# Kernel tuning notes

Measured on AMD Instinct MI355X. Metric: run time of the kernel, lower is better.

Reference implementation:

```python
import jax, jax.numpy as jnp
import numpy as np

IN_CH, OUT_CH, Z1, B = 794, 512, 1024, 32768


def _build_masks(rng):
    # MADE connectivity masks, same construction as the torch module
    m0 = np.concatenate([np.ones(10, dtype=np.int64), np.arange(1, 785)])  # len 794
    m1 = rng.integers(1, IN_CH, size=Z1)
    m2 = rng.integers(m1.min(), IN_CH, size=OUT_CH)
    MW0 = (m1[:, None] >= m0[None, :IN_CH]).astype(np.float32)  # [Z1, IN_CH]
    MW1 = (m2[:, None] >= m1[None, :]).astype(np.float32)        # [OUT_CH, Z1]
    return jnp.asarray(MW0), jnp.asarray(MW1)


def setup_inputs() -> dict:
    key = jax.random.key(0)
    ks = jax.random.split(key, 9)
    s1 = 1.0 / np.sqrt(IN_CH)
    s2 = 1.0 / np.sqrt(Z1)
    MW0, MW1 = _build_masks(np.random.default_rng(0))
    return {
        "x":   jax.random.normal(ks[0], (B, IN_CH), dtype=jnp.float32),
        "W1":  jax.random.uniform(ks[1], (Z1, IN_CH), jnp.float32, -s1, s1),
        "b1":  jax.random.uniform(ks[2], (Z1,), jnp.float32, -s1, s1),
        "Wc1": jax.random.uniform(ks[3], (Z1, IN_CH), jnp.float32, -s1, s1),
        "bc1": jax.random.uniform(ks[4], (Z1,), jnp.float32, -s1, s1),
        "W2":  jax.random.uniform(ks[5], (OUT_CH, Z1), jnp.float32, -s2, s2),
        "b2":  jax.random.uniform(ks[6], (OUT_CH,), jnp.float32, -s2, s2),
        "Wc2": jax.random.uniform(ks[7], (OUT_CH, Z1), jnp.float32, -s2, s2),
        "bc2": jax.random.uniform(ks[8], (OUT_CH,), jnp.float32, -s2, s2),
        "MW0": MW0,
        "MW1": MW1,
    }


def reference(x, W1, b1, Wc1, bc1, W2, b2, Wc2, bc2, MW0, MW1):
    # F.linear(ones_like(x), Wc, bc) == row-sum of masked Wc + bc (same math, no GEMM)
    mW1, mWc1 = W1 * MW0, Wc1 * MW0
    h1 = jax.nn.relu(x @ mW1.T + b1 + jnp.sum(mWc1, axis=1) + bc1)  # [B, Z1]
    mW2, mWc2 = W2 * MW1, Wc2 * MW1
    h2 = jax.nn.relu(h1 @ mW2.T + b2 + jnp.sum(mWc2, axis=1) + bc2)  # [B, OUT_CH]
    return h2
```

## Files before the change

### kernel.cpp

```cpp
#include <hip/hip_runtime.h>
#include <hip/hip_bf16.h>
#include <stdint.h>

#define IN_CH 794
#define KPAD  832
#define Z1C   1024
#define OUT_C 512
#define BATCH 32768

typedef __attribute__((ext_vector_type(8))) short short8;
typedef __attribute__((ext_vector_type(4))) float f32x4;

__device__ __forceinline__ ushort f2bf(float f) {
  uint32_t u = __float_as_uint(f);
  return (ushort)((u + 0x7fffu + ((u >> 16) & 1u)) >> 16);
}

__device__ __forceinline__ void glds16(const void* g, void* l) {
  __builtin_amdgcn_global_load_lds(
      (const __attribute__((address_space(1))) void*)g,
      (__attribute__((address_space(3))) void*)l, 16, 0, 0);
}

#define BAR() __builtin_amdgcn_s_barrier()
#define MFMA(a, b, c) __builtin_amdgcn_mfma_f32_16x16x32_bf16(a, b, c, 0, 0, 0)

__global__ __launch_bounds__(256) void prep1(
    const float* __restrict__ W1, const float* __restrict__ b1,
    const float* __restrict__ Wc1, const float* __restrict__ bc1,
    const float* __restrict__ MW0, ushort* __restrict__ w1p,
    float* __restrict__ bias1) {
  int z = blockIdx.x, t = threadIdx.x;
  float sum = 0.f;
  for (int i = t; i < KPAD; i += 256) {
    float w = 0.f;
    if (i < IN_CH) {
      float m = MW0[z * IN_CH + i];
      w = W1[z * IN_CH + i] * m;
      sum += Wc1[z * IN_CH + i] * m;
    }
    w1p[z * KPAD + i] = f2bf(w);
  }
#pragma unroll
  for (int o = 32; o > 0; o >>= 1) sum += __shfl_down(sum, o, 64);
  __shared__ float red[4];
  if ((t & 63) == 0) red[t >> 6] = sum;
  __syncthreads();
  if (t == 0) bias1[z] = b1[z] + bc1[z] + red[0] + red[1] + red[2] + red[3];
}

__global__ __launch_bounds__(256) void prep2(
    const float* __restrict__ W2, const float* __restrict__ b2,
    const float* __restrict__ Wc2, const float* __restrict__ bc2,
    const float* __restrict__ MW1, ushort* __restrict__ w2m,
    float* __restrict__ bias2) {
  int z = blockIdx.x, t = threadIdx.x;
  float sum = 0.f;
  for (int i = t; i < Z1C; i += 256) {
    float m = MW1[z * Z1C + i];
    w2m[z * Z1C + i] = f2bf(W2[z * Z1C + i] * m);
    sum += Wc2[z * Z1C + i] * m;
  }
#pragma unroll
  for (int o = 32; o > 0; o >>= 1) sum += __shfl_down(sum, o, 64);
  __shared__ float red[4];
  if ((t & 63) == 0) red[t >> 6] = sum;
  __syncthreads();
  if (t == 0) bias2[z] = b2[z] + bc2[z] + red[0] + red[1] + red[2] + red[3];
}

__global__ __launch_bounds__(256) void xcvt(const float* __restrict__ x,
                                            ushort* __restrict__ xb) {
  const int CPR = KPAD / 8;
  const int total = BATCH * CPR;
  for (int i = blockIdx.x * 256 + threadIdx.x; i < total;
       i += gridDim.x * 256) {
    int row = i / CPR;
    int col = (i - row * CPR) * 8;
    const float* p = x + (size_t)row * IN_CH + col;
    ushort u[8];
    if (col + 8 <= IN_CH) {
#pragma unroll
      for (int j = 0; j < 4; ++j) {
        float2 v = *(const float2*)(p + j * 2);
        u[j * 2] = f2bf(v.x);
        u[j * 2 + 1] = f2bf(v.y);
      }
    } else {
#pragma unroll
      for (int j = 0; j < 8; ++j) u[j] = (col + j < IN_CH) ? f2bf(p[j]) : 0;
    }
    *(uint4*)(xb + (size_t)row * KPAD + col) = *(uint4*)u;
  }
}

template <int KP, int NKT, int NCB, int OSTR, bool BF16OUT>
__global__ __launch_bounds__(512, 2) void gemm8(
    const ushort* __restrict__ Ag, const ushort* __restrict__ Bg,
    const float* __restrict__ bias, void* __restrict__ Cout) {
  __shared__ ushort lds[73728];
  char* const L = (char*)lds;
  const int tid = threadIdx.x;
  const int lane = tid & 63, wid = tid >> 6;
  const int wr = wid >> 1, wc = wid & 1;

  const int nwg = gridDim.x;
  const int w0 = blockIdx.x;
  const int swz = (w0 & 7) * (nwg >> 3) + (w0 >> 3);
  const int bcol = (swz % NCB) * 128;
  const int brow = (swz / NCB) * 256;

  const int ra0 = tid >> 3;
  const int ra1 = 64 + (tid >> 3);
  const int cbs = (tid & 7) * 16;
  const size_t gA0 = (size_t)(brow + ra0) * (KP * 2) + (cbs ^ ((ra0 & 7) << 4));
  const size_t gA1 = (size_t)(brow + ra1) * (KP * 2) + (cbs ^ ((ra1 & 7) << 4));
  const int rb = tid >> 3;
  const size_t gB = (size_t)(bcol + rb) * (KP * 2) + (cbs ^ ((rb & 7) << 4));

  auto stA0 = [&](char* bufp, int kt, int h) {
    glds16((const char*)Ag + gA0 + (size_t)h * (128 * KP * 2) + (size_t)kt * 128,
           bufp + h * 16384 + wid * 1024);
  };
  auto stA1 = [&](char* bufp, int kt, int h) {
    glds16((const char*)Ag + gA1 + (size_t)h * (128 * KP * 2) + (size_t)kt * 128,
           bufp + h * 16384 + 8192 + wid * 1024);
  };
  auto stB = [&](char* bufp, int kt, int h) {
    glds16((const char*)Bg + gB + (size_t)h * (64 * KP * 2) + (size_t)kt * 128,
           bufp + 32768 + h * 8192 + wid * 1024);
  };

  const int rA = lane & 15;
  const int klo = (lane >> 4) * 16;
  const int xs = (rA & 7) << 4;

  f32x4 acc[4][4] = {};

  {
    char* b0 = L;
    stA0(b0, 0, 0); stA1(b0, 0, 0); stA0(b0, 0, 1); stA1(b0, 0, 1);
    stB(b0, 0, 0); stB(b0, 0, 1);
    char* b1 = L + 49152;
    stA0(b1, 1, 0); stA1(b1, 1, 0); stA0(b1, 1, 1); stA1(b1, 1, 1);
    stB(b1, 1, 0); stB(b1, 1, 1);
  }
  asm volatile("s_waitcnt vmcnt(6)" ::: "memory");
  BAR();

  for (int j = 0; j < NKT; ++j) {
    char* const Lb = L + (j % 3) * 49152;
    const bool pf = (j + 2 < NKT);
    char* const L2 = L + ((j + 2) % 3) * 49152;
    const int j2 = j + 2;

    auto rdA = [&](int m, int ks) -> short8 {
      int lrow = (wr & 1) * 64 + m * 16 + rA;
      return *(const short8*)(Lb + (wr >> 1) * 16384 + lrow * 128 +
                              ((ks * 64 + klo) ^ xs));
    };
    auto rdB = [&](int n, int ks) -> short8 {
      return *(const short8*)(Lb + 32768 + wc * 8192 + (n * 16 + rA) * 128 +
                              ((ks * 64 + klo) ^ xs));
    };

    short8 a0k0 = rdA(0, 0), a0k1 = rdA(0, 1);
    short8 a1k0 = rdA(1, 0), a1k1 = rdA(1, 1);
    short8 b0k0 = rdB(0, 0), b0k1 = rdB(0, 1);
    short8 b1k0 = rdB(1, 0), b1k1 = rdB(1, 1);
    if (pf) { stA0(L2, j2, 0); stA1(L2, j2, 0); }
    BAR();
    __builtin_amdgcn_s_setprio(1);
    acc[0][0] = MFMA(a0k0, b0k0, acc[0][0]); acc[0][0] = MFMA(a0k1, b0k1, acc[0][0]);
    acc[0][1] = MFMA(a0k0, b1k0, acc[0][1]); acc[0][1] = MFMA(a0k1, b1k1, acc[0][1]);
    acc[1][0] = MFMA(a1k0, b0k0, acc[1][0]); acc[1][0] = MFMA(a1k1, b0k1, acc[1][0]);
    acc[1][1] = MFMA(a1k0, b1k0, acc[1][1]); acc[1][1] = MFMA(a1k1, b1k1, acc[1][1]);
    __builtin_amdgcn_s_setprio(0);
    BAR();

    short8 b2k0 = rdB(2, 0), b2k1 = rdB(2, 1);
    short8 b3k0 = rdB(3, 0), b3k1 = rdB(3, 1);
    if (pf) { stA0(L2, j2, 1); stA1(L2, j2, 1); }
    BAR();
    __builtin_amdgcn_s_setprio(1);
    acc[0][2] = MFMA(a0k0, b2k0, acc[0][2]); acc[0][2] = MFMA(a0k1, b2k1, acc[0][2]);
    acc[0][3] = MFMA(a0k0, b3k0, acc[0][3]); acc[0][3] = MFMA(a0k1, b3k1, acc[0][3]);
    acc[1][2] = MFMA(a1k0, b2k0, acc[1][2]); acc[1][2] = MFMA(a1k1, b2k1, acc[1][2]);
    acc[1][3] = MFMA(a1k0, b3k0, acc[1][3]); acc[1][3] = MFMA(a1k1, b3k1, acc[1][3]);
    __builtin_amdgcn_s_setprio(0);
    BAR();

    short8 a2k0 = rdA(2, 0), a2k1 = rdA(2, 1);
    short8 a3k0 = rdA(3, 0), a3k1 = rdA(3, 1);
    if (pf) stB(L2, j2, 0);
    BAR();
    __builtin_amdgcn_s_setprio(1);
    acc[2][0] = MFMA(a2k0, b0k0, acc[2][0]); acc[2][0] = MFMA(a2k1, b0k1, acc[2][0]);
    acc[2][1] = MFMA(a2k0, b1k0, acc[2][1]); acc[2][1] = MFMA(a2k1, b1k1, acc[2][1]);
    acc[3][0] = MFMA(a3k0, b0k0, acc[3][0]); acc[3][0] = MFMA(a3k1, b0k1, acc[3][0]);
    acc[3][1] = MFMA(a3k0, b1k0, acc[3][1]); acc[3][1] = MFMA(a3k1, b1k1, acc[3][1]);
    __builtin_amdgcn_s_setprio(0);
    BAR();

    if (pf) {
      stB(L2, j2, 1);
      asm volatile("s_waitcnt vmcnt(6)" ::: "memory");
    } else if (j + 1 < NKT) {
      asm volatile("s_waitcnt vmcnt(0)" ::: "memory");
    }
    BAR();
    __builtin_amdgcn_s_setprio(1);
    acc[2][2] = MFMA(a2k0, b2k0, acc[2][2]); acc[2][2] = MFMA(a2k1, b2k1, acc[2][2]);
    acc[2][3] = MFMA(a2k0, b3k0, acc[2][3]); acc[2][3] = MFMA(a2k1, b3k1, acc[2][3]);
    acc[3][2] = MFMA(a3k0, b2k0, acc[3][2]); acc[3][2] = MFMA(a3k1, b2k1, acc[3][2]);
    acc[3][3] = MFMA(a3k0, b3k0, acc[3][3]); acc[3][3] = MFMA(a3k1, b3k1, acc[3][3]);
    __builtin_amdgcn_s_setprio(0);
    BAR();
  }

#pragma unroll
  for (int n = 0; n < 4; ++n) {
    const int col = bcol + wc * 64 + n * 16 + rA;
    const float bv = bias[col];
#pragma unroll
    for (int m = 0; m < 4; ++m) {
#pragma unroll
      for (int r = 0; r < 4; ++r) {
        const int row = brow + wr * 64 + m * 16 + (lane >> 4) * 4 + r;
        float v = acc[m][n][r] + bv;
        v = v > 0.f ? v : 0.f;
        if (BF16OUT)
          ((ushort*)Cout)[(size_t)row * OSTR + col] = f2bf(v);
        else
          ((float*)Cout)[(size_t)row * OSTR + col] = v;
      }
    }
  }
}

__global__ __launch_bounds__(256, 2) void gemm1_fused(
    const float* __restrict__ x, const ushort* __restrict__ w1p,
    const float* __restrict__ bias1, ushort* __restrict__ h1) {
  __shared__ ushort As[128 * 32];
  __shared__ ushort Bs[128 * 32];
  const int tid = threadIdx.x;
  const int lane = tid & 63, wid = tid >> 6;
  const int wr = wid >> 1, wc = wid & 1;
  const int brow = blockIdx.x * 128;
  const int bcol = blockIdx.y * 128;

  f32x4 acc[4][4] = {};
  const int arow = tid >> 1;
  const int acol0 = (tid & 1) * 16;
  const float* xrow = x + (size_t)(brow + arow) * IN_CH;

  for (int kt = 0; kt < 26; ++kt) {
    const int k0 = kt * 32;
#pragma unroll
    for (int c = 0; c < 2; ++c) {
      int idx16 = (wid * 2 + c) * 64 + lane;
      int row = idx16 >> 2, chunk = idx16 & 3;
      glds16(w1p + (size_t)(bcol + row) * KPAD + k0 + chunk * 8,
             (char*)Bs + (wid * 2 + c) * 1024);
    }
    union { ushort u[16]; uint4 q[2]; } pk;
    if (kt < 24) {
      const float* p = xrow + k0 + acol0;
#pragma unroll
      for (int j = 0; j < 8; ++j) {
        float2 v = *(const float2*)(p + j * 2);
        pk.u[j * 2] = f2bf(v.x);
        pk.u[j * 2 + 1] = f2bf(v.y);
      }
    } else {
#pragma unroll
      for (int j = 0; j < 16; ++j) {
        int col = k0 + acol0 + j;
        pk.u[j] = f2bf(col < IN_CH ? xrow[col] : 0.f);
      }
    }
    *(uint4*)&As[arow * 32 + acol0] = pk.q[0];
    *(uint4*)&As[arow * 32 + acol0 + 8] = pk.q[1];

    __syncthreads();
    const int kb = (lane >> 4) * 8, rA = lane & 15;
    short8 af[4], bfrag[4];
#pragma unroll
    for (int m = 0; m < 4; ++m)
      af[m] = *(const short8*)&As[(wr * 64 + m * 16 + rA) * 32 + kb];
#pragma unroll
    for (int n = 0; n < 4; ++n)
      bfrag[n] = *(const short8*)&Bs[(wc * 64 + n * 16 + rA) * 32 + kb];
#pragma unroll
    for (int m = 0; m < 4; ++m)
#pragma unroll
      for (int n = 0; n < 4; ++n)
        acc[m][n] = MFMA(af[m], bfrag[n], acc[m][n]);
    __syncthreads();
  }

  const int orow0 = brow + wr * 64;
  const int ocol0 = bcol + wc * 64;
#pragma unroll
  for (int n = 0; n < 4; ++n) {
    int col = ocol0 + n * 16 + (lane & 15);
    float bv = bias1[col];
#pragma unroll
    for (int m = 0; m < 4; ++m)
#pragma unroll
      for (int r = 0; r < 4; ++r) {
        int row = orow0 + m * 16 + (lane >> 4) * 4 + r;
        float v = acc[m][n][r] + bv;
        v = v > 0.f ? v : 0.f;
        h1[(size_t)row * Z1C + col] = f2bf(v);
      }
  }
}

extern "C" void kernel_launch(void* const* d_in, const int* in_sizes, int n_in,
                              void* d_out, int out_size, void* d_ws, size_t ws_size,
                              hipStream_t stream) {
  (void)in_sizes; (void)n_in; (void)out_size;
  const float* x   = (const float*)d_in[0];
  const float* W1  = (const float*)d_in[1];
  const float* b1  = (const float*)d_in[2];
  const float* Wc1 = (const float*)d_in[3];
  const float* bc1 = (const float*)d_in[4];
  const float* W2  = (const float*)d_in[5];
  const float* b2  = (const float*)d_in[6];
  const float* Wc2 = (const float*)d_in[7];
  const float* bc2 = (const float*)d_in[8];
  const float* MW0 = (const float*)d_in[9];
  const float* MW1 = (const float*)d_in[10];

  char* ws = (char*)d_ws;
  ushort* w1p   = (ushort*)ws;
  ushort* w2m   = (ushort*)(ws + 1703936);
  float*  bias1 = (float*)(ws + 2752512);
  float*  bias2 = (float*)(ws + 2756608);
  ushort* xb    = (ushort*)(ws + 2758656);
  const size_t WS_NEED = 2758656ull + 54525952ull;

  ushort* h1 = (ushort*)d_out;
  float*  out = (float*)d_out;

  prep1<<<1024, 256, 0, stream>>>(W1, b1, Wc1, bc1, MW0, w1p, bias1);
  prep2<<<512, 256, 0, stream>>>(W2, b2, Wc2, bc2, MW1, w2m, bias2);

  if (ws_size >= WS_NEED) {
    xcvt<<<2048, 256, 0, stream>>>(x, xb);
    gemm8<KPAD, 13, 8, Z1C, true><<<1024, 512, 0, stream>>>(xb, w1p, bias1, h1);
  } else {
    gemm1_fused<<<dim3(256, 8), 256, 0, stream>>>(x, w1p, bias1, h1);
  }
  gemm8<Z1C, 16, 4, OUT_C, false><<<512, 512, 0, stream>>>(h1, w2m, bias2, out);
}
```

Baseline: 140.1 us.

## Enlarge GEMM block tile to 256x256 with 2x4 warp layout and split buffering

Replaces the 256x128 block tile with a 256x256 tile, arranging 8 waves as 2x4 with each wave computing 128x64 (8x4 MFMA accumulators). A uses a triple-buffered LDS ring and B a double buffer, with loads interleaved into four compute phases. The aim is higher arithmetic intensity per LDS byte and fewer global reloads of operand tiles. In exchange it doubles accumulator registers and raises LDS use to 160KB, which may limit occupancy to one block per CU despite the launch bounds, and halves the grid size.

```diff
diff --git a/kernel.cpp b/kernel.cpp
--- a/kernel.cpp
+++ b/kernel.cpp
@@ -95,126 +95,137 @@
 }
 
 template <int KP, int NKT, int NCB, int OSTR, bool BF16OUT>
-__global__ __launch_bounds__(512, 2) void gemm8(
+__global__ __launch_bounds__(512, 2) void gemmT(
     const ushort* __restrict__ Ag, const ushort* __restrict__ Bg,
     const float* __restrict__ bias, void* __restrict__ Cout) {
-  __shared__ ushort lds[73728];
-  char* const L = (char*)lds;
+  __shared__ uint4 ldsq[10240];
+  char* const L = (char*)ldsq;
+  char* const LB = L + 98304;
   const int tid = threadIdx.x;
   const int lane = tid & 63, wid = tid >> 6;
-  const int wr = wid >> 1, wc = wid & 1;
+  const int wr = wid >> 2, wc = wid & 3;
 
   const int nwg = gridDim.x;
   const int w0 = blockIdx.x;
   const int swz = (w0 & 7) * (nwg >> 3) + (w0 >> 3);
-  const int bcol = (swz % NCB) * 128;
+  const int bcol = (swz % NCB) * 256;
   const int brow = (swz / NCB) * 256;
 
-  const int ra0 = tid >> 3;
-  const int ra1 = 64 + (tid >> 3);
-  const int cbs = (tid & 7) * 16;
-  const size_t gA0 = (size_t)(brow + ra0) * (KP * 2) + (cbs ^ ((ra0 & 7) << 4));
-  const size_t gA1 = (size_t)(brow + ra1) * (KP * 2) + (cbs ^ ((ra1 & 7) << 4));
-  const int rb = tid >> 3;
-  const size_t gB = (size_t)(bcol + rb) * (KP * 2) + (cbs ^ ((rb & 7) << 4));
-
-  auto stA0 = [&](char* bufp, int kt, int h) {
-    glds16((const char*)Ag + gA0 + (size_t)h * (128 * KP * 2) + (size_t)kt * 128,
-           bufp + h * 16384 + wid * 1024);
+  const int srow = tid >> 3;
+  const int scol = ((tid & 7) * 16) ^ ((srow & 7) << 4);
+  const char* gAp = (const char*)Ag + (size_t)(brow + srow) * (KP * 2) + scol;
+  const char* gBp = (const char*)Bg + (size_t)(bcol + srow) * (KP * 2) + scol;
+  const int ldst = wid * 1024;
+
+  auto stA = [&](int buf, int kt, int h) {
+    glds16(gAp + (size_t)h * (64 * KP * 2) + (size_t)kt * 128,
+           L + buf * 32768 + h * 8192 + ldst);
   };
-  auto stA1 = [&](char* bufp, int kt, int h) {
-    glds16((const char*)Ag + gA1 + (size_t)h * (128 * KP * 2) + (size_t)kt * 128,
-           bufp + h * 16384 + 8192 + wid * 1024);
-  };
-  auto stB = [&](char* bufp, int kt, int h) {
-    glds16((const char*)Bg + gB + (size_t)h * (64 * KP * 2) + (size_t)kt * 128,
-           bufp + 32768 + h * 8192 + wid * 1024);
+  auto stB = [&](int buf, int kt, int h) {
+    glds16(gBp + (size_t)h * (64 * KP * 2) + (size_t)kt * 128,
+           LB + buf * 32768 + h * 8192 + ldst);
   };
 
   const int rA = lane & 15;
   const int klo = (lane >> 4) * 16;
   const int xs = (rA & 7) << 4;
-
-  f32x4 acc[4][4] = {};
-
-  {
-    char* b0 = L;
-    stA0(b0, 0, 0); stA1(b0, 0, 0); stA0(b0, 0, 1); stA1(b0, 0, 1);
-    stB(b0, 0, 0); stB(b0, 0, 1);
-    char* b1 = L + 49152;
-    stA0(b1, 1, 0); stA1(b1, 1, 0); stA0(b1, 1, 1); stA1(b1, 1, 1);
-    stB(b1, 1, 0); stB(b1, 1, 1);
-  }
-  asm volatile("s_waitcnt vmcnt(6)" ::: "memory");
+  auto rdA = [&](const char* Ab, int m, int ks) -> short8 {
+    int row = wr * 128 + m * 16 + rA;
+    return *(const short8*)(Ab + row * 128 + ((ks * 64 + klo) ^ xs));
+  };
+  auto rdB = [&](const char* Bb, int n, int ks) -> short8 {
+    int row = wc * 64 + n * 16 + rA;
+    return *(const short8*)(Bb + row * 128 + ((ks * 64 + klo) ^ xs));
+  };
+
+  f32x4 acc[8][4] = {};
+
+#pragma unroll
+  for (int h = 0; h < 4; ++h) stA(0, 0, h);
+#pragma unroll
+  for (int h = 0; h < 4; ++h) stB(0, 0, h);
+#pragma unroll
+  for (int h = 0; h < 4; ++h) stA(1, 1, h);
+  asm volatile("s_waitcnt vmcnt(4)" ::: "memory");
   BAR();
 
   for (int j = 0; j < NKT; ++j) {
-    char* const Lb = L + (j % 3) * 49152;
-    const bool pf = (j + 2 < NKT);
-    char* const L2 = L + ((j + 2) % 3) * 49152;
-    const int j2 = j + 2;
-
-    auto rdA = [&](int m, int ks) -> short8 {
-      int lrow = (wr & 1) * 64 + m * 16 + rA;
-      return *(const short8*)(Lb + (wr >> 1) * 16384 + lrow * 128 +
-                              ((ks * 64 + klo) ^ xs));
-    };
-    auto rdB = [&](int n, int ks) -> short8 {
-      return *(const short8*)(Lb + 32768 + wc * 8192 + (n * 16 + rA) * 128 +
-                              ((ks * 64 + klo) ^ xs));
-    };
-
-    short8 a0k0 = rdA(0, 0), a0k1 = rdA(0, 1);
-    short8 a1k0 = rdA(1, 0), a1k1 = rdA(1, 1);
-    short8 b0k0 = rdB(0, 0), b0k1 = rdB(0, 1);
-    short8 b1k0 = rdB(1, 0), b1k1 = rdB(1, 1);
-    if (pf) { stA0(L2, j2, 0); stA1(L2, j2, 0); }
+    const char* Ab = L + (j % 3) * 32768;
+    const char* Bb = LB + (j & 1) * 32768;
+    const int jn = j + 1, ja = j + 2;
+    const int bb1 = jn & 1, ab2 = ja % 3;
+    short8 aF[4][2], bF[4][2];
+
+#pragma unroll
+    for (int m = 0; m < 4; ++m) {
+      aF[m][0] = rdA(Ab, m, 0); aF[m][1] = rdA(Ab, m, 1);
+    }
+#pragma unroll
+    for (int n = 0; n < 2; ++n) {
+      bF[n][0] = rdB(Bb, n, 0); bF[n][1] = rdB(Bb, n, 1);
+    }
+    if (jn < NKT) { stB(bb1, jn, 0); stB(bb1, jn, 1); }
     BAR();
     __builtin_amdgcn_s_setprio(1);
-    acc[0][0] = MFMA(a0k0, b0k0, acc[0][0]); acc[0][0] = MFMA(a0k1, b0k1, acc[0][0]);
-    acc[0][1] = MFMA(a0k0, b1k0, acc[0][1]); acc[0][1] = MFMA(a0k1, b1k1, acc[0][1]);
-    acc[1][0] = MFMA(a1k0, b0k0, acc[1][0]); acc[1][0] = MFMA(a1k1, b0k1, acc[1][0]);
-    acc[1][1] = MFMA(a1k0, b1k0, acc[1][1]); acc[1][1] = MFMA(a1k1, b1k1, acc[1][1]);
+#pragma unroll
+    for (int ks = 0; ks < 2; ++ks)
+#pragma unroll
+      for (int m = 0; m < 4; ++m)
+#pragma unroll
+        for (int n = 0; n < 2; ++n)
+          acc[m][n] = MFMA(aF[m][ks], bF[n][ks], acc[m][n]);
     __builtin_amdgcn_s_setprio(0);
     BAR();
 
-    short8 b2k0 = rdB(2, 0), b2k1 = rdB(2, 1);
-    short8 b3k0 = rdB(3, 0), b3k1 = rdB(3, 1);
-    if (pf) { stA0(L2, j2, 1); stA1(L2, j2, 1); }
+#pragma unroll
+    for (int n = 2; n < 4; ++n) {
+      bF[n][0] = rdB(Bb, n, 0); bF[n][1] = rdB(Bb, n, 1);
+    }
+    if (jn < NKT) { stB(bb1, jn, 2); stB(bb1, jn, 3); }
     BAR();
     __builtin_amdgcn_s_setprio(1);
-    acc[0][2] = MFMA(a0k0, b2k0, acc[0][2]); acc[0][2] = MFMA(a0k1, b2k1, acc[0][2]);
-    acc[0][3] = MFMA(a0k0, b3k0, acc[0][3]); acc[0][3] = MFMA(a0k1, b3k1, acc[0][3]);
-    acc[1][2] = MFMA(a1k0, b2k0, acc[1][2]); acc[1][2] = MFMA(a1k1, b2k1, acc[1][2]);
-    acc[1][3] = MFMA(a1k0, b3k0, acc[1][3]); acc[1][3] = MFMA(a1k1, b3k1, acc[1][3]);
+#pragma unroll
+    for (int ks = 0; ks < 2; ++ks)
+#pragma unroll
+      for (int m = 0; m < 4; ++m)
+#pragma unroll
+        for (int n = 2; n < 4; ++n)
+          acc[m][n] = MFMA(aF[m][ks], bF[n][ks], acc[m][n]);
     __builtin_amdgcn_s_setprio(0);
     BAR();
 
-    short8 a2k0 = rdA(2, 0), a2k1 = rdA(2, 1);
-    short8 a3k0 = rdA(3, 0), a3k1 = rdA(3, 1);
-    if (pf) stB(L2, j2, 0);
+#pragma unroll
+    for (int m = 0; m < 4; ++m) {
+      aF[m][0] = rdA(Ab, m + 4, 0); aF[m][1] = rdA(Ab, m + 4, 1);
+    }
+    if (ja < NKT) { stA(ab2, ja, 0); stA(ab2, ja, 1); }
     BAR();
     __builtin_amdgcn_s_setprio(1);
-    acc[2][0] = MFMA(a2k0, b0k0, acc[2][0]); acc[2][0] = MFMA(a2k1, b0k1, acc[2][0]);
-    acc[2][1] = MFMA(a2k0, b1k0, acc[2][1]); acc[2][1] = MFMA(a2k1, b1k1, acc[2][1]);
-    acc[3][0] = MFMA(a3k0, b0k0, acc[3][0]); acc[3][0] = MFMA(a3k1, b0k1, acc[3][0]);
-    acc[3][1] = MFMA(a3k0, b1k0, acc[3][1]); acc[3][1] = MFMA(a3k1, b1k1, acc[3][1]);
+#pragma unroll
+    for (int ks = 0; ks < 2; ++ks)
+#pragma unroll
+      for (int m = 0; m < 4; ++m)
+#pragma unroll
+        for (int n = 0; n < 2; ++n)
+          acc[m + 4][n] = MFMA(aF[m][ks], bF[n][ks], acc[m + 4][n]);
     __builtin_amdgcn_s_setprio(0);
     BAR();
 
-    if (pf) {
-      stB(L2, j2, 1);
-      asm volatile("s_waitcnt vmcnt(6)" ::: "memory");
-    } else if (j + 1 < NKT) {
+    if (ja < NKT) { stA(ab2, ja, 2); stA(ab2, ja, 3); }
+    BAR();
+    __builtin_amdgcn_s_setprio(1);
+#pragma unroll
+    for (int ks = 0; ks < 2; ++ks)
+#pragma unroll
+      for (int m = 0; m < 4; ++m)
+#pragma unroll
+        for (int n = 2; n < 4; ++n)
+          acc[m + 4][n] = MFMA(aF[m][ks], bF[n][ks], acc[m + 4][n]);
+    __builtin_amdgcn_s_setprio(0);
+    if (ja < NKT)
+      asm volatile("s_waitcnt vmcnt(4)" ::: "memory");
+    else if (jn < NKT)
       asm volatile("s_waitcnt vmcnt(0)" ::: "memory");
-    }
-    BAR();
-    __builtin_amdgcn_s_setprio(1);
-    acc[2][2] = MFMA(a2k0, b2k0, acc[2][2]); acc[2][2] = MFMA(a2k1, b2k1, acc[2][2]);
-    acc[2][3] = MFMA(a2k0, b3k0, acc[2][3]); acc[2][3] = MFMA(a2k1, b3k1, acc[2][3]);
-    acc[3][2] = MFMA(a3k0, b2k0, acc[3][2]); acc[3][2] = MFMA(a3k1, b2k1, acc[3][2]);
-    acc[3][3] = MFMA(a3k0, b3k0, acc[3][3]); acc[3][3] = MFMA(a3k1, b3k1, acc[3][3]);
-    __builtin_amdgcn_s_setprio(0);
     BAR();
   }
 
@@ -223,10 +234,10 @@
     const int col = bcol + wc * 64 + n * 16 + rA;
     const float bv = bias[col];
 #pragma unroll
-    for (int m = 0; m < 4; ++m) {
+    for (int m = 0; m < 8; ++m) {
 #pragma unroll
       for (int r = 0; r < 4; ++r) {
-        const int row = brow + wr * 64 + m * 16 + (lane >> 4) * 4 + r;
+        const int row = brow + wr * 128 + m * 16 + (lane >> 4) * 4 + r;
         float v = acc[m][n][r] + bv;
         v = v > 0.f ? v : 0.f;
         if (BF16OUT)
@@ -349,9 +360,9 @@
 
   if (ws_size >= WS_NEED) {
     xcvt<<<2048, 256, 0, stream>>>(x, xb);
-    gemm8<KPAD, 13, 8, Z1C, true><<<1024, 512, 0, stream>>>(xb, w1p, bias1, h1);
+    gemmT<KPAD, 13, 4, Z1C, true><<<512, 512, 0, stream>>>(xb, w1p, bias1, h1);
   } else {
     gemm1_fused<<<dim3(256, 8), 256, 0, stream>>>(x, w1p, bias1, h1);
   }
-  gemm8<Z1C, 16, 4, OUT_C, false><<<512, 512, 0, stream>>>(h1, w2m, bias2, out);
-}
+  gemmT<Z1C, 16, 2, OUT_C, false><<<256, 512, 0, stream>>>(h1, w2m, bias2, out);
+}
```

New measurement: 140.1 us. About the same (+0.0%).
